# Performance work log

Measured on AMD Instinct MI355X. Metric: run time of the kernel, lower is better.

## Reference

```python
import jax, jax.numpy as jnp
import numpy as np

N_HEADS = 16
LOCAL_WINDOW = 256
GLOBAL_WINDOW = 1024


def _block_mha(x, in_proj_w, in_proj_b, out_proj_w, out_proj_b, window, n_heads):
    """Non-overlapping sliding-window MHA, matching torch nn.MultiheadAttention math.

    x: [B, S, D]; windows are independent -> fold them into the batch dim and do
    one batched attention (block-diagonal attention over the sequence).
    """
    B, S, D = x.shape
    nw = S // window
    hd = D // n_heads
    xw = x.reshape(B * nw, window, D)
    # combined QKV projection: in_proj_w is [3D, D], torch applies x @ W^T + b
    qkv = xw @ in_proj_w.T + in_proj_b  # [B*nw, W, 3D]
    q, k, v = jnp.split(qkv, 3, axis=-1)
    q = q.reshape(B * nw, window, n_heads, hd)
    k = k.reshape(B * nw, window, n_heads, hd)
    v = v.reshape(B * nw, window, n_heads, hd)
    scale = 1.0 / np.sqrt(hd).astype(np.float32)
    scores = jnp.einsum('bqhd,bkhd->bhqk', q, k) * scale
    attn = jax.nn.softmax(scores, axis=-1)
    out = jnp.einsum('bhqk,bkhd->bqhd', attn, v).reshape(B * nw, window, D)
    out = out @ out_proj_w.T + out_proj_b
    return out.reshape(B, S, D)


def setup_inputs() -> dict:
    key = jax.random.key(0)
    ks = jax.random.split(key, 8)
    B, S, D = 2, 4096, 1024
    w_scale = 1.0 / np.sqrt(D).astype(np.float32)
    return {
        'lqs': jax.random.normal(ks[0], (B, S, D), dtype=jnp.float32),
        'gqs': jax.random.normal(ks[1], (B, S, D), dtype=jnp.float32),
        'in_proj_w_l': jax.random.normal(ks[2], (3 * D, D), dtype=jnp.float32) * w_scale,
        'in_proj_b_l': jnp.zeros((3 * D,), dtype=jnp.float32),
        'out_proj_w_l': jax.random.normal(ks[3], (D, D), dtype=jnp.float32) * w_scale,
        'out_proj_b_l': jnp.zeros((D,), dtype=jnp.float32),
        'in_proj_w_g': jax.random.normal(ks[4], (3 * D, D), dtype=jnp.float32) * w_scale,
        'in_proj_b_g': jnp.zeros((3 * D,), dtype=jnp.float32),
        'out_proj_w_g': jax.random.normal(ks[5], (D, D), dtype=jnp.float32) * w_scale,
        'out_proj_b_g': jnp.zeros((D,), dtype=jnp.float32),
    }


def reference(lqs, gqs, in_proj_w_l, in_proj_b_l, out_proj_w_l, out_proj_b_l,
              in_proj_w_g, in_proj_b_g, out_proj_w_g, out_proj_b_g):
    local_out = _block_mha(lqs, in_proj_w_l, in_proj_b_l, out_proj_w_l, out_proj_b_l,
                           LOCAL_WINDOW, N_HEADS)
    global_out = _block_mha(gqs, in_proj_w_g, in_proj_b_g, out_proj_w_g, out_proj_b_g,
                            GLOBAL_WINDOW, N_HEADS)
    return (local_out, global_out)
```

## Files before the change

kernel.cpp:

```cpp
#include <hip/hip_runtime.h>
#include <stdint.h>

typedef __attribute__((ext_vector_type(8))) __bf16 bf16x8;
typedef __attribute__((ext_vector_type(4))) float f32x4;

__device__ __forceinline__ void async_ld16(const void* g, void* l) {
  __builtin_amdgcn_global_load_lds(
      (const __attribute__((address_space(1))) unsigned int*)g,
      (__attribute__((address_space(3))) unsigned int*)l, 16, 0, 0);
}

__device__ __forceinline__ unsigned short f2bf(float x) {
  union { float f; unsigned int u; } v; v.f = x;
  unsigned int r = v.u + 0x7FFFu + ((v.u >> 16) & 1u);
  return (unsigned short)(r >> 16);
}

__device__ __forceinline__ float exp2_fast(float x) {
  return __builtin_amdgcn_exp2f(x);
}

__device__ __forceinline__ unsigned int pack_bf2(float a, float b) {
  unsigned int ua = __builtin_bit_cast(unsigned int, a) + 0x8000u;
  unsigned int ub = __builtin_bit_cast(unsigned int, b) + 0x8000u;
  return __builtin_amdgcn_perm(ub, ua, 0x07060302u);
}

__global__ void cvt_f32_bf16(const float* __restrict__ src,
                             unsigned short* __restrict__ dst, int n4) {
  int i = blockIdx.x * blockDim.x + threadIdx.x;
  if (i >= n4) return;
  float4 v = ((const float4*)src)[i];
  ushort4 o;
  o.x = f2bf(v.x); o.y = f2bf(v.y); o.z = f2bf(v.z); o.w = f2bf(v.w);
  ((ushort4*)dst)[i] = o;
}

__global__ __launch_bounds__(256)
void gemm_bt(const unsigned short* __restrict__ A,
             const unsigned short* __restrict__ B,
             const float* __restrict__ bias,
             void* __restrict__ outp, int N, int K, int f32out,
             int qlim, float qs) {
  __shared__ unsigned short As[128 * 64];
  __shared__ unsigned short Bs[128 * 64];
  int tid = threadIdx.x;
  int wave = tid >> 6, lane = tid & 63;
  int quad = lane >> 4, l16 = lane & 15;
  int wm = (wave >> 1) * 64, wn = (wave & 1) * 64;
  size_t bm = (size_t)blockIdx.y * 128, bn = (size_t)blockIdx.x * 128;

  f32x4 zero = {0.f, 0.f, 0.f, 0.f};
  f32x4 acc[4][4];
  for (int i = 0; i < 4; i++)
    for (int j = 0; j < 4; j++) acc[i][j] = zero;

  int swz = l16 & 7;

  for (int k0 = 0; k0 < K; k0 += 64) {
    __syncthreads();
#pragma unroll
    for (int j = 0; j < 4; j++) {
      int c = j * 256 + tid;
      int row = c >> 3, sl = c & 7, ss = sl ^ (row & 7);
      async_ld16(A + (bm + row) * K + k0 + ss * 8, (char*)As + c * 16);
      async_ld16(B + (bn + row) * K + k0 + ss * 8, (char*)Bs + c * 16);
    }
    __syncthreads();

    bf16x8 bfr[4][2];
#pragma unroll
    for (int i = 0; i < 4; i++)
#pragma unroll
      for (int ch = 0; ch < 2; ch++) {
        int sl = (ch * 4 + quad) ^ swz;
        bfr[i][ch] = *(const bf16x8*)&Bs[(wn + i * 16 + l16) * 64 + sl * 8];
      }
#pragma unroll
    for (int mi = 0; mi < 4; mi++) {
      bf16x8 af[2];
#pragma unroll
      for (int ch = 0; ch < 2; ch++) {
        int sl = (ch * 4 + quad) ^ swz;
        af[ch] = *(const bf16x8*)&As[(wm + mi * 16 + l16) * 64 + sl * 8];
      }
#pragma unroll
      for (int ni = 0; ni < 4; ni++) {
        acc[mi][ni] = __builtin_amdgcn_mfma_f32_16x16x32_bf16(
            bfr[ni][0], af[0], acc[mi][ni], 0, 0, 0);
        acc[mi][ni] = __builtin_amdgcn_mfma_f32_16x16x32_bf16(
            bfr[ni][1], af[1], acc[mi][ni], 0, 0, 0);
      }
    }
  }

#pragma unroll
  for (int mi = 0; mi < 4; mi++) {
    size_t rowg = bm + wm + mi * 16 + l16;
#pragma unroll
    for (int ni = 0; ni < 4; ni++) {
      size_t col = bn + wn + ni * 16 + quad * 4;
      float s = ((int)col < qlim) ? qs : 1.0f;
      float4 bv = *(const float4*)&bias[col];
      f32x4 a = acc[mi][ni];
      if (f32out) {
        float4 o = {(a[0] + bv.x) * s, (a[1] + bv.y) * s,
                    (a[2] + bv.z) * s, (a[3] + bv.w) * s};
        *(float4*)&((float*)outp)[rowg * N + col] = o;
      } else {
        ushort4 o;
        o.x = f2bf((a[0] + bv.x) * s); o.y = f2bf((a[1] + bv.y) * s);
        o.z = f2bf((a[2] + bv.z) * s); o.w = f2bf((a[3] + bv.w) * s);
        *(ushort4*)&((unsigned short*)outp)[rowg * N + col] = o;
      }
    }
  }
}

__device__ __forceinline__ int kperm(int p) {
  return (p & 0xC3) | ((p & 0x0C) << 2) | ((p & 0x30) >> 2);
}
__global__ void transpose_v(const unsigned short* __restrict__ qkv,
                            unsigned short* __restrict__ vt, int W) {
  __shared__ unsigned short tile[64][33];
  int wb = blockIdx.z;
  int c0 = blockIdx.x * 32, w0 = blockIdx.y * 64;
  const unsigned short* src = qkv + (size_t)wb * W * 3072 + 2048;
  for (int i = threadIdx.y; i < 64; i += 8)
    tile[i][threadIdx.x] = src[(size_t)(w0 + i) * 3072 + c0 + threadIdx.x];
  __syncthreads();
  unsigned short* dst = vt + (size_t)wb * 1024 * W;
  for (int i = threadIdx.y; i < 32; i += 8) {
    int p0 = threadIdx.x, p1 = threadIdx.x + 32;
    dst[(size_t)(c0 + i) * W + w0 + p0] = tile[kperm(p0)][i];
    dst[(size_t)(c0 + i) * W + w0 + p1] = tile[kperm(p1)][i];
  }
}

__global__ __launch_bounds__(256)
void attn_fused(const unsigned short* __restrict__ qkv,
                const unsigned short* __restrict__ vt,
                unsigned short* __restrict__ ao, int W) {
  __shared__ unsigned short Ks[64 * 64];
  __shared__ unsigned short Vs[64 * 64];
  __shared__ unsigned int   Ps[4][16 * 32];
  int tid = threadIdx.x;
  int wave = tid >> 6, lane = tid & 63;
  int quad = lane >> 4, l16 = lane & 15;
  int swz = l16 & 7;
  int wbh = blockIdx.y;
  int wb = wbh >> 4, h = wbh & 15;
  int q0w = blockIdx.x * 128 + wave * 32;

  const unsigned short* qb = qkv + (size_t)wb * W * 3072 + h * 64;
  const unsigned short* kb = qb + 1024;
  const unsigned short* vtb = vt + (size_t)wbh * 64 * W;

  bf16x8 qf[2][2];
  for (int cb = 0; cb < 2; cb++)
    for (int ch = 0; ch < 2; ch++)
      qf[cb][ch] = *(const bf16x8*)(qb + (size_t)(q0w + cb * 16 + l16) * 3072 +
                                    ch * 32 + quad * 8);

  f32x4 zero = {0.f, 0.f, 0.f, 0.f};
  f32x4 O[2][4];
  for (int cb = 0; cb < 2; cb++)
    for (int g = 0; g < 4; g++) O[cb][g] = zero;
  float l_i[2] = {0.f, 0.f};

  for (int k0 = 0; k0 < W; k0 += 64) {
    __syncthreads();
    for (int j = 0; j < 2; j++) {
      int c = j * 256 + tid;
      int row = c >> 3, sl = c & 7, ss = sl ^ (row & 7);
      async_ld16(kb + (size_t)(k0 + row) * 3072 + ss * 8, (char*)Ks + c * 16);
      async_ld16(vtb + (size_t)row * W + k0 + ss * 8,     (char*)Vs + c * 16);
    }
    __syncthreads();

    bf16x8 ak[4][2], vf[4][2];
#pragma unroll
    for (int i = 0; i < 4; i++)
#pragma unroll
      for (int ch = 0; ch < 2; ch++) {
        int sl = (ch * 4 + quad) ^ swz;
        ak[i][ch] = *(const bf16x8*)&Ks[(i * 16 + l16) * 64 + sl * 8];
        vf[i][ch] = *(const bf16x8*)&Vs[(i * 16 + l16) * 64 + sl * 8];
      }

    for (int cb = 0; cb < 2; cb++) {
      unsigned int pk[8];
      float sm = 0.f;
#pragma unroll
      for (int sub = 0; sub < 4; sub++) {
        f32x4 z = zero;
        z = __builtin_amdgcn_mfma_f32_16x16x32_bf16(ak[sub][0], qf[cb][0], z, 0, 0, 0);
        z = __builtin_amdgcn_mfma_f32_16x16x32_bf16(ak[sub][1], qf[cb][1], z, 0, 0, 0);
        float p0 = exp2_fast(z[0]), p1 = exp2_fast(z[1]);
        float p2 = exp2_fast(z[2]), p3 = exp2_fast(z[3]);
        sm += (p0 + p1) + (p2 + p3);
        pk[((sub & 1) * 2) + (sub >> 1) * 4]     = pack_bf2(p0, p1);
        pk[((sub & 1) * 2) + (sub >> 1) * 4 + 1] = pack_bf2(p2, p3);
      }
      sm += __shfl_xor(sm, 16);
      sm += __shfl_xor(sm, 32);
      l_i[cb] += sm;

      unsigned int* pw = &Ps[wave][0];
      uint4 u0 = {pk[0], pk[1], pk[2], pk[3]};
      uint4 u1 = {pk[4], pk[5], pk[6], pk[7]};
      *(uint4*)&pw[l16 * 32 + ((2 * quad) ^ swz) * 4]     = u0;
      *(uint4*)&pw[l16 * 32 + ((2 * quad + 1) ^ swz) * 4] = u1;

      bf16x8 pf[2];
#pragma unroll
      for (int ch = 0; ch < 2; ch++) {
        uint4 u = *(const uint4*)&pw[l16 * 32 + ((ch * 4 + quad) ^ swz) * 4];
        pf[ch] = __builtin_bit_cast(bf16x8, u);
      }
#pragma unroll
      for (int g = 0; g < 4; g++) {
        O[cb][g] = __builtin_amdgcn_mfma_f32_16x16x32_bf16(pf[0], vf[g][0], O[cb][g], 0, 0, 0);
        O[cb][g] = __builtin_amdgcn_mfma_f32_16x16x32_bf16(pf[1], vf[g][1], O[cb][g], 0, 0, 0);
      }
    }
  }

  for (int cb = 0; cb < 2; cb++) {
    float inv = 1.0f / l_i[cb];
    float ivr[4];
    for (int r = 0; r < 4; r++) ivr[r] = __shfl(inv, quad * 4 + r);
    for (int r = 0; r < 4; r++) {
      size_t rowg = (size_t)wb * W + q0w + cb * 16 + quad * 4 + r;
      for (int g = 0; g < 4; g++)
        ao[rowg * 1024 + h * 64 + g * 16 + l16] = f2bf(O[cb][g][r] * ivr[r]);
    }
  }
}

extern "C" void kernel_launch(void* const* d_in, const int* in_sizes, int n_in,
                              void* d_out, int out_size, void* d_ws, size_t ws_size,
                              hipStream_t stream) {
  const int D = 1024, TD = 3072, M = 8192, NH = 16;
  const float QS = 0.125f * 1.44269504089f;
  unsigned short* Xb  = (unsigned short*)d_ws;
  unsigned short* Wb  = Xb + 8388608;
  unsigned short* Ob  = Wb + 3145728;
  unsigned short* qkv = Ob + 1048576;
  unsigned short* vt  = qkv + 25165824;
  float* outp = (float*)d_out;

  for (int br = 0; br < 2; br++) {
    const float* x   = (const float*)d_in[br];
    const float* ipw = (const float*)d_in[2 + 4 * br];
    const float* ipb = (const float*)d_in[3 + 4 * br];
    const float* opw = (const float*)d_in[4 + 4 * br];
    const float* opb = (const float*)d_in[5 + 4 * br];
    int W = (br == 0) ? 256 : 1024;
    int nwb = M / W;

    cvt_f32_bf16<<<8192, 256, 0, stream>>>(x, Xb, 8388608 / 4);
    cvt_f32_bf16<<<3072, 256, 0, stream>>>(ipw, Wb, 3145728 / 4);
    cvt_f32_bf16<<<1024, 256, 0, stream>>>(opw, Ob, 1048576 / 4);

    gemm_bt<<<dim3(TD / 128, M / 128), 256, 0, stream>>>(
        Xb, Wb, ipb, qkv, TD, D, 0, D, QS);

    transpose_v<<<dim3(32, W / 64, nwb), dim3(32, 8), 0, stream>>>(qkv, vt, W);

    attn_fused<<<dim3(W / 128, nwb * NH), 256, 0, stream>>>(qkv, vt, Xb, W);

    gemm_bt<<<dim3(D / 128, M / 128), 256, 0, stream>>>(
        Xb, Ob, opb, outp + (size_t)br * 8388608, D, D, 1, 0, 1.0f);
  }
}
```

Baseline: 483.5 us.

## Batch local and global branches into shared launches with merged conversions

When the workspace is large enough, each branch gets its own buffers, and both branches run through single launches of the QKV GEMM, V transpose, attention and output GEMM. The grid gains a branch dimension or a flattened block index. The three f32-to-bf16 conversions per branch are merged into one kernel, and the GEMM load addresses are precomputed and advanced by pointer increments. The aim is fewer launches, fewer small under-filled grids, and overlap of the uneven branch workloads, at the cost of twice the workspace and more index logic per block.

Result: faster. 460.4 us (-4.8%).

```diff
diff --git a/kernel.cpp b/kernel.cpp
--- a/kernel.cpp
+++ b/kernel.cpp
@@ -26,24 +26,34 @@
   return __builtin_amdgcn_perm(ub, ua, 0x07060302u);
 }
 
-__global__ void cvt_f32_bf16(const float* __restrict__ src,
-                             unsigned short* __restrict__ dst, int n4) {
-  int i = blockIdx.x * blockDim.x + threadIdx.x;
-  if (i >= n4) return;
-  float4 v = ((const float4*)src)[i];
+__global__ void cvt3(const float* __restrict__ x, unsigned short* __restrict__ xd,
+                     const float* __restrict__ w1, unsigned short* __restrict__ w1d,
+                     const float* __restrict__ w2, unsigned short* __restrict__ w2d) {
+  int i = blockIdx.x * 256 + threadIdx.x;
+  const float* s; unsigned short* d; int off;
+  if (i < 2097152)      { s = x;  d = xd;  off = i; }
+  else if (i < 2883584) { s = w1; d = w1d; off = i - 2097152; }
+  else                  { s = w2; d = w2d; off = i - 2883584; }
+  float4 v = ((const float4*)s)[off];
   ushort4 o;
   o.x = f2bf(v.x); o.y = f2bf(v.y); o.z = f2bf(v.z); o.w = f2bf(v.w);
-  ((ushort4*)dst)[i] = o;
+  ((ushort4*)d)[off] = o;
 }
 
 __global__ __launch_bounds__(256)
-void gemm_bt(const unsigned short* __restrict__ A,
-             const unsigned short* __restrict__ B,
-             const float* __restrict__ bias,
-             void* __restrict__ outp, int N, int K, int f32out,
-             int qlim, float qs) {
+void gemm_bt(const unsigned short* __restrict__ A0, const unsigned short* __restrict__ A1,
+             const unsigned short* __restrict__ B0, const unsigned short* __restrict__ B1,
+             const float* __restrict__ bias0, const float* __restrict__ bias1,
+             void* __restrict__ out0, void* __restrict__ out1,
+             int N, int K, int f32out, int qlim, float qs) {
   __shared__ unsigned short As[128 * 64];
   __shared__ unsigned short Bs[128 * 64];
+  int br = blockIdx.z;
+  const unsigned short* A = br ? A1 : A0;
+  const unsigned short* B = br ? B1 : B0;
+  const float* bias = br ? bias1 : bias0;
+  void* outp = br ? out1 : out0;
+
   int tid = threadIdx.x;
   int wave = tid >> 6, lane = tid & 63;
   int quad = lane >> 4, l16 = lane & 15;
@@ -57,14 +67,23 @@
 
   int swz = l16 & 7;
 
+  const unsigned short* ap[4];
+#pragma unroll
+  for (int j = 0; j < 4; j++) {
+    int c = j * 256 + tid;
+    int row = c >> 3, ss = (c & 7) ^ (row & 7);
+    ap[j] = A + (bm + row) * K + ss * 8;
+  }
+  const ptrdiff_t dB = (B + bn * (size_t)K) - (A + bm * (size_t)K);
+
   for (int k0 = 0; k0 < K; k0 += 64) {
     __syncthreads();
 #pragma unroll
     for (int j = 0; j < 4; j++) {
       int c = j * 256 + tid;
-      int row = c >> 3, sl = c & 7, ss = sl ^ (row & 7);
-      async_ld16(A + (bm + row) * K + k0 + ss * 8, (char*)As + c * 16);
-      async_ld16(B + (bn + row) * K + k0 + ss * 8, (char*)Bs + c * 16);
+      async_ld16(ap[j],      (char*)As + c * 16);
+      async_ld16(ap[j] + dB, (char*)Bs + c * 16);
+      ap[j] += 64;
     }
     __syncthreads();
 
@@ -120,11 +139,15 @@
 __device__ __forceinline__ int kperm(int p) {
   return (p & 0xC3) | ((p & 0x0C) << 2) | ((p & 0x30) >> 2);
 }
-__global__ void transpose_v(const unsigned short* __restrict__ qkv,
-                            unsigned short* __restrict__ vt, int W) {
+__global__ void transpose_v(const unsigned short* __restrict__ q0, unsigned short* __restrict__ v0, int W0,
+                            const unsigned short* __restrict__ q1, unsigned short* __restrict__ v1, int W1,
+                            int zsplit) {
   __shared__ unsigned short tile[64][33];
-  int wb = blockIdx.z;
-  int c0 = blockIdx.x * 32, w0 = blockIdx.y * 64;
+  int z = blockIdx.z;
+  const unsigned short* qkv; unsigned short* vt; int W, wb, yy;
+  if (z < zsplit) { qkv = q0; vt = v0; W = W0; wb = z; yy = blockIdx.y; }
+  else { qkv = q1; vt = v1; W = W1; int t = z - zsplit; wb = t >> 2; yy = blockIdx.y + 4 * (t & 3); }
+  int c0 = blockIdx.x * 32, w0 = yy * 64;
   const unsigned short* src = qkv + (size_t)wb * W * 3072 + 2048;
   for (int i = threadIdx.y; i < 64; i += 8)
     tile[i][threadIdx.x] = src[(size_t)(w0 + i) * 3072 + c0 + threadIdx.x];
@@ -138,23 +161,32 @@
 }
 
 __global__ __launch_bounds__(256)
-void attn_fused(const unsigned short* __restrict__ qkv,
-                const unsigned short* __restrict__ vt,
-                unsigned short* __restrict__ ao, int W) {
+void attn_fused(const unsigned short* __restrict__ qkv0, const unsigned short* __restrict__ vt0,
+                unsigned short* __restrict__ ao0, int W0, int nb0,
+                const unsigned short* __restrict__ qkv1, const unsigned short* __restrict__ vt1,
+                unsigned short* __restrict__ ao1, int W1) {
   __shared__ unsigned short Ks[64 * 64];
   __shared__ unsigned short Vs[64 * 64];
   __shared__ unsigned int   Ps[4][16 * 32];
+  int bid = blockIdx.x;
+  const unsigned short *qkv, *vtb0; unsigned short* ao; int W, rel;
+  if (bid < nb0) { qkv = qkv0; vtb0 = vt0; ao = ao0; W = W0; rel = bid; }
+  else           { qkv = qkv1; vtb0 = vt1; ao = ao1; W = W1; rel = bid - nb0; }
+  int gx = W >> 7;
+  int shift = (gx == 2) ? 1 : 3;
+  int bx = rel & (gx - 1);
+  int wbh = rel >> shift;
+  int wb = wbh >> 4, h = wbh & 15;
+
   int tid = threadIdx.x;
   int wave = tid >> 6, lane = tid & 63;
   int quad = lane >> 4, l16 = lane & 15;
   int swz = l16 & 7;
-  int wbh = blockIdx.y;
-  int wb = wbh >> 4, h = wbh & 15;
-  int q0w = blockIdx.x * 128 + wave * 32;
+  int q0w = bx * 128 + wave * 32;
 
   const unsigned short* qb = qkv + (size_t)wb * W * 3072 + h * 64;
   const unsigned short* kb = qb + 1024;
-  const unsigned short* vtb = vt + (size_t)wbh * 64 * W;
+  const unsigned short* vtb = vtb0 + (size_t)wbh * 64 * W;
 
   bf16x8 qf[2][2];
   for (int cb = 0; cb < 2; cb++)
@@ -241,36 +273,62 @@
 extern "C" void kernel_launch(void* const* d_in, const int* in_sizes, int n_in,
                               void* d_out, int out_size, void* d_ws, size_t ws_size,
                               hipStream_t stream) {
-  const int D = 1024, TD = 3072, M = 8192, NH = 16;
+  const int D = 1024, TD = 3072, M = 8192;
   const float QS = 0.125f * 1.44269504089f;
-  unsigned short* Xb  = (unsigned short*)d_ws;
-  unsigned short* Wb  = Xb + 8388608;
-  unsigned short* Ob  = Wb + 3145728;
-  unsigned short* qkv = Ob + 1048576;
-  unsigned short* vt  = qkv + 25165824;
+  const size_t PER = 46137344;
+  bool comb = ws_size >= (size_t)2 * PER * 2;
+
+  unsigned short* Xb[2]; unsigned short* Wb[2]; unsigned short* Ob[2];
+  unsigned short* qkv[2]; unsigned short* vt[2];
+  for (int b = 0; b < 2; b++) {
+    unsigned short* base = (unsigned short*)d_ws + (comb ? b * PER : 0);
+    Xb[b]  = base;
+    Wb[b]  = Xb[b] + 8388608;
+    Ob[b]  = Wb[b] + 3145728;
+    qkv[b] = Ob[b] + 1048576;
+    vt[b]  = qkv[b] + 25165824;
+  }
   float* outp = (float*)d_out;
-
-  for (int br = 0; br < 2; br++) {
-    const float* x   = (const float*)d_in[br];
-    const float* ipw = (const float*)d_in[2 + 4 * br];
-    const float* ipb = (const float*)d_in[3 + 4 * br];
-    const float* opw = (const float*)d_in[4 + 4 * br];
-    const float* opb = (const float*)d_in[5 + 4 * br];
-    int W = (br == 0) ? 256 : 1024;
-    int nwb = M / W;
-
-    cvt_f32_bf16<<<8192, 256, 0, stream>>>(x, Xb, 8388608 / 4);
-    cvt_f32_bf16<<<3072, 256, 0, stream>>>(ipw, Wb, 3145728 / 4);
-    cvt_f32_bf16<<<1024, 256, 0, stream>>>(opw, Ob, 1048576 / 4);
-
-    gemm_bt<<<dim3(TD / 128, M / 128), 256, 0, stream>>>(
-        Xb, Wb, ipb, qkv, TD, D, 0, D, QS);
-
-    transpose_v<<<dim3(32, W / 64, nwb), dim3(32, 8), 0, stream>>>(qkv, vt, W);
-
-    attn_fused<<<dim3(W / 128, nwb * NH), 256, 0, stream>>>(qkv, vt, Xb, W);
-
-    gemm_bt<<<dim3(D / 128, M / 128), 256, 0, stream>>>(
-        Xb, Ob, opb, outp + (size_t)br * 8388608, D, D, 1, 0, 1.0f);
-  }
-}
+  const float* x[2]   = {(const float*)d_in[0], (const float*)d_in[1]};
+  const float* ipw[2] = {(const float*)d_in[2], (const float*)d_in[6]};
+  const float* ipb[2] = {(const float*)d_in[3], (const float*)d_in[7]};
+  const float* opw[2] = {(const float*)d_in[4], (const float*)d_in[8]};
+  const float* opb[2] = {(const float*)d_in[5], (const float*)d_in[9]};
+  const int Wd[2] = {256, 1024};
+
+  if (comb) {
+    for (int b = 0; b < 2; b++)
+      cvt3<<<12288, 256, 0, stream>>>(x[b], Xb[b], ipw[b], Wb[b], opw[b], Ob[b]);
+    gemm_bt<<<dim3(TD / 128, M / 128, 2), 256, 0, stream>>>(
+        Xb[0], Xb[1], Wb[0], Wb[1], ipb[0], ipb[1], qkv[0], qkv[1],
+        TD, D, 0, D, QS);
+    transpose_v<<<dim3(32, 4, 64), dim3(32, 8), 0, stream>>>(
+        qkv[0], vt[0], 256, qkv[1], vt[1], 1024, 32);
+    attn_fused<<<2048, 256, 0, stream>>>(
+        qkv[0], vt[0], Xb[0], 256, 1024, qkv[1], vt[1], Xb[1], 1024);
+    gemm_bt<<<dim3(D / 128, M / 128, 2), 256, 0, stream>>>(
+        Xb[0], Xb[1], Ob[0], Ob[1], opb[0], opb[1], outp, outp + 8388608,
+        D, D, 1, 0, 1.0f);
+  } else {
+    for (int b = 0; b < 2; b++) {
+      int W = Wd[b], nwb = M / W;
+      cvt3<<<12288, 256, 0, stream>>>(x[b], Xb[b], ipw[b], Wb[b], opw[b], Ob[b]);
+      gemm_bt<<<dim3(TD / 128, M / 128, 1), 256, 0, stream>>>(
+          Xb[b], Xb[b], Wb[b], Wb[b], ipb[b], ipb[b], qkv[b], qkv[b],
+          TD, D, 0, D, QS);
+      if (b == 0)
+        transpose_v<<<dim3(32, 4, 32), dim3(32, 8), 0, stream>>>(
+            qkv[b], vt[b], W, qkv[b], vt[b], W, 32);
+      else
+        transpose_v<<<dim3(32, 4, 32), dim3(32, 8), 0, stream>>>(
+            qkv[b], vt[b], W, qkv[b], vt[b], W, 0);
+      int nb = (W >> 7) * nwb * 16;
+      attn_fused<<<nb, 256, 0, stream>>>(
+          qkv[b], vt[b], Xb[b], W, nb, qkv[b], vt[b], Xb[b], W);
+      gemm_bt<<<dim3(D / 128, M / 128, 1), 256, 0, stream>>>(
+          Xb[b], Xb[b], Ob[b], Ob[b], opb[b], opb[b],
+          outp + (size_t)b * 8388608, outp + (size_t)b * 8388608,
+          D, D, 1, 0, 1.0f);
+    }
+  }
+}
```
